# Performance work log

Hardware: AMD Instinct MI355X
Metric: run time of the kernel (lower is better)

Reference implementation:

```python
import jax, jax.numpy as jnp
import numpy as np
from jax import lax

B, L = 8, 2048
TOP_K = 30
NUM_RBF = 16
NUM_POS = 16
NODE_IN, EDGE_IN = 6, NUM_POS + NUM_RBF  # features_type='dist'
H = 128  # node_features == edge_features


def setup_inputs() -> dict:
    key = jax.random.key(0)
    ks = jax.random.split(key, 4)
    # coords scaled so pairwise distances span the RBF range [0, 20]
    X = jax.random.normal(ks[0], (B, L, 4, 3), dtype=jnp.float32) * 10.0
    mask = jnp.ones((B, L), dtype=jnp.float32)
    W_node = jax.random.normal(ks[1], (NODE_IN, H), dtype=jnp.float32) * 0.1
    b_node = jnp.zeros((H,), dtype=jnp.float32)
    W_edge = jax.random.normal(ks[2], (EDGE_IN, H), dtype=jnp.float32) * 0.1
    b_edge = jnp.zeros((H,), dtype=jnp.float32)
    gamma_n = jnp.ones((H,), dtype=jnp.float32)
    beta_n = jnp.zeros((H,), dtype=jnp.float32)
    gamma_e = jnp.ones((H,), dtype=jnp.float32)
    beta_e = jnp.zeros((H,), dtype=jnp.float32)
    return {"X": X, "mask": mask, "W_node": W_node, "b_node": b_node,
            "W_edge": W_edge, "b_edge": b_edge, "gamma_n": gamma_n,
            "beta_n": beta_n, "gamma_e": gamma_e, "beta_e": beta_e}


def _dist(X_ca, mask, eps=1e-6):
    # masked pairwise Euclidean distances + kNN (smallest)
    mask_2D = mask[:, None, :] * mask[:, :, None]            # [B,L,L]
    dX = X_ca[:, None, :, :] - X_ca[:, :, None, :]           # [B,L,L,3]
    D = mask_2D * jnp.sqrt(jnp.sum(dX * dX, axis=-1) + eps)  # [B,L,L]
    D_max = jnp.max(D, axis=-1, keepdims=True)
    D_adjust = D + (1.0 - mask_2D) * (D_max + 1.0)
    neg_D, E_idx = lax.top_k(-D_adjust, TOP_K)               # smallest-k
    return -neg_D, E_idx                                     # [B,L,K], [B,L,K]


def _rbf(D):
    D_mu = jnp.linspace(0.0, 20.0, NUM_RBF)                  # [R]
    D_sigma = 20.0 / NUM_RBF
    return jnp.exp(-(((D[..., None] - D_mu) / D_sigma) ** 2))  # [B,L,K,R]


def _positional_encodings(E_idx):
    # directional differential positional encodings
    N_nodes = E_idx.shape[1]
    ii = jnp.arange(N_nodes, dtype=jnp.float32)[None, :, None]
    d = (E_idx.astype(jnp.float32) - ii)[..., None]          # [B,L,K,1]
    freq = jnp.exp(jnp.arange(0, NUM_POS, 2, dtype=jnp.float32)
                   * (-(np.log(10000.0) / NUM_POS)))          # [P/2]
    angles = d * freq                                        # [B,L,K,P/2]
    return jnp.concatenate([jnp.cos(angles), jnp.sin(angles)], axis=-1)


def _dihedrals(X, eps=1e-7):
    # phi/psi/omega from N,CA,C backbone trace -> [B,L,6]
    b, n = X.shape[0], X.shape[1]
    Xb = X[:, :, :3, :].reshape(b, 3 * n, 3)
    dX = Xb[:, 1:, :] - Xb[:, :-1, :]
    U = dX / (jnp.linalg.norm(dX, axis=-1, keepdims=True) + 1e-8)
    u_2, u_1, u_0 = U[:, :-2], U[:, 1:-1], U[:, 2:]
    n_2 = jnp.cross(u_2, u_1)
    n_2 = n_2 / (jnp.linalg.norm(n_2, axis=-1, keepdims=True) + 1e-8)
    n_1 = jnp.cross(u_1, u_0)
    n_1 = n_1 / (jnp.linalg.norm(n_1, axis=-1, keepdims=True) + 1e-8)
    cosD = jnp.clip(jnp.sum(n_2 * n_1, axis=-1), -1.0 + eps, 1.0 - eps)
    Dang = jnp.sign(jnp.sum(u_2 * n_1, axis=-1)) * jnp.arccos(cosD)
    Dang = jnp.pad(Dang, ((0, 0), (1, 2)))
    Dang = Dang.reshape(b, n, 3)
    return jnp.concatenate([jnp.cos(Dang), jnp.sin(Dang)], axis=-1)


def _layer_norm(x, gamma, beta, eps=1e-5):
    mu = jnp.mean(x, axis=-1, keepdims=True)
    var = jnp.mean((x - mu) ** 2, axis=-1, keepdims=True)
    return (x - mu) * lax.rsqrt(var + eps) * gamma + beta


def reference(X, mask, W_node, b_node, W_edge, b_edge,
              gamma_n, beta_n, gamma_e, beta_e):
    X_ca = X[:, :, 1, :]
    D_neighbors, E_idx = _dist(X_ca, mask)
    E_positional = _positional_encodings(E_idx)              # [B,L,K,P]
    RBF = _rbf(D_neighbors)                                  # [B,L,K,R]
    V = _dihedrals(X)                                        # [B,L,6]
    E = jnp.concatenate([E_positional, RBF], axis=-1)        # [B,L,K,P+R]
    V = _layer_norm(V @ W_node + b_node, gamma_n, beta_n)
    E = _layer_norm(E @ W_edge + b_edge, gamma_e, beta_e)
    return V, E, E_idx
```

## Files before the change

### kernel.cpp

```cpp
#include <hip/hip_runtime.h>
#include <cstdint>
#include <cstddef>

#define NB 8
#define NL 2048
#define TOPK 30
#define NH 128
#define CAND_CAP 256
#define EDGE_BLOCKS 1920
#define EDGE_WAVES (EDGE_BLOCKS * 4)

typedef unsigned long long ull;
typedef __attribute__((ext_vector_type(8))) short short8v;
typedef __attribute__((ext_vector_type(4))) float f32x4;

__device__ __forceinline__ short f2bf(float f) {
    unsigned int b = __float_as_uint(f);
    b += 0x7fffu + ((b >> 16) & 1u);
    return (short)(b >> 16);
}

__global__ __launch_bounds__(512) void topk_kernel(
    const float* __restrict__ X, const float* __restrict__ mask,
    float* __restrict__ eidx, float* __restrict__ dnb)
{
    __shared__ float4 Ps[NL];
    __shared__ ull cand[8][CAND_CAP];

    const int tid = threadIdx.x;
    const int wv  = tid >> 6;
    const int ln  = tid & 63;
    const int row = blockIdx.x * 8 + wv;
    const int b   = row >> 11;
    const int i   = row & (NL - 1);

    const float* Xb = X + (size_t)b * NL * 12;
    const float* Mb = mask + (size_t)b * NL;
    #pragma unroll
    for (int q = 0; q < 4; ++q) {
        const int j = tid + 512 * q;
        const float* x = Xb + (size_t)j * 12 + 3;
        Ps[j] = make_float4(x[0], x[1], x[2], Mb[j]);
    }
    __syncthreads();

    const float4 pi = Ps[i];
    const float xi = pi.x, yi = pi.y, zi = pi.z, mi = pi.w;

    unsigned int u[32];
    float lm0 = 0.0f, lm1 = 0.0f, lm2 = 0.0f, lm3 = 0.0f;
    #pragma unroll
    for (int t = 0; t < 32; t += 4) {
        #pragma unroll
        for (int q = 0; q < 4; ++q) {
            const float4 pj = Ps[ln + 64 * (t + q)];
            float dx = xi - pj.x;
            float dy = yi - pj.y;
            float dz = zi - pj.z;
            float s = __fadd_rn(__fmul_rn(dx, dx), __fmul_rn(dy, dy));
            s = __fadd_rn(s, __fmul_rn(dz, dz));
            s = __fadd_rn(s, 1e-6f);
            float m2 = __fmul_rn(pj.w, mi);
            float d  = __fmul_rn(m2, __fsqrt_rn(s));
            u[t + q] = __float_as_uint(d) | ((m2 == 0.0f) ? 0x80000000u : 0u);
            if      (q == 0) lm0 = fmaxf(lm0, d);
            else if (q == 1) lm1 = fmaxf(lm1, d);
            else if (q == 2) lm2 = fmaxf(lm2, d);
            else             lm3 = fmaxf(lm3, d);
        }
    }
    float lmax = fmaxf(fmaxf(lm0, lm1), fmaxf(lm2, lm3));
    #pragma unroll
    for (int off = 32; off; off >>= 1) lmax = fmaxf(lmax, __shfl_xor(lmax, off));
    const unsigned int DMB = __float_as_uint(__fadd_rn(lmax, 1.0f));

    unsigned int um0 = 0xFFFFFFFFu, um1 = 0xFFFFFFFFu,
                 um2 = 0xFFFFFFFFu, um3 = 0xFFFFFFFFu;
    #pragma unroll
    for (int t = 0; t < 32; t += 4) {
        unsigned int b0 = (u[t+0] & 0x80000000u) ? DMB : u[t+0];
        unsigned int b1 = (u[t+1] & 0x80000000u) ? DMB : u[t+1];
        unsigned int b2 = (u[t+2] & 0x80000000u) ? DMB : u[t+2];
        unsigned int b3 = (u[t+3] & 0x80000000u) ? DMB : u[t+3];
        u[t+0] = b0; u[t+1] = b1; u[t+2] = b2; u[t+3] = b3;
        um0 = min(um0, b0); um1 = min(um1, b1);
        um2 = min(um2, b2); um3 = min(um3, b3);
    }
    unsigned int umin = min(min(um0, um1), min(um2, um3));

    unsigned int v = umin;
    #pragma unroll
    for (int k = 2; k <= 64; k <<= 1) {
        #pragma unroll
        for (int j = k >> 1; j > 0; j >>= 1) {
            unsigned int o = __shfl_xor(v, j);
            bool asc   = ((ln & k) == 0);
            bool lower = ((ln & j) == 0);
            v = (lower == asc) ? min(v, o) : max(v, o);
        }
    }
    const unsigned int T = __shfl(v, TOPK - 1);

    unsigned int base = 0;
    #pragma unroll
    for (int t = 0; t < 32; ++t) {
        bool act = u[t] <= T;
        ull m = __ballot(act);
        if (act) {
            unsigned int pos = base + (unsigned)__popcll(m & ((1ull << ln) - 1ull));
            if (pos < CAND_CAP)
                cand[wv][pos] = ((ull)u[t] << 32) | (unsigned)(ln + 64 * t);
        }
        base += (unsigned)__popcll(m);
    }
    const unsigned int cnt = base;

    float* eo  = eidx + (size_t)row * TOPK;
    float* dno = dnb  + (size_t)row * TOPK;

    if (cnt <= CAND_CAP) {
        ull k0 = ((unsigned)ln        < cnt) ? cand[wv][ln]        : ~0ULL;
        ull k1 = ((unsigned)ln +  64u < cnt) ? cand[wv][ln +  64]  : ~0ULL;
        ull k2 = ((unsigned)ln + 128u < cnt) ? cand[wv][ln + 128]  : ~0ULL;
        ull k3 = ((unsigned)ln + 192u < cnt) ? cand[wv][ln + 192]  : ~0ULL;
        int r0 = 0, r1 = 0, r2 = 0, r3 = 0;
        for (unsigned int p = 0; p < cnt; p += 4) {
            ull c0 = cand[wv][p];
            ull c1 = (p + 1 < cnt) ? cand[wv][p + 1] : ~0ULL;
            ull c2 = (p + 2 < cnt) ? cand[wv][p + 2] : ~0ULL;
            ull c3 = (p + 3 < cnt) ? cand[wv][p + 3] : ~0ULL;
            r0 += (c0 < k0) + (c1 < k0) + (c2 < k0) + (c3 < k0);
            r1 += (c0 < k1) + (c1 < k1) + (c2 < k1) + (c3 < k1);
            r2 += (c0 < k2) + (c1 < k2) + (c2 < k2) + (c3 < k2);
            r3 += (c0 < k3) + (c1 < k3) + (c2 < k3) + (c3 < k3);
        }
        if (r0 < TOPK) { eo[r0] = (float)(unsigned)(k0 & 0xFFFFFFFFu); dno[r0] = __uint_as_float((unsigned)(k0 >> 32)); }
        if (r1 < TOPK) { eo[r1] = (float)(unsigned)(k1 & 0xFFFFFFFFu); dno[r1] = __uint_as_float((unsigned)(k1 >> 32)); }
        if (r2 < TOPK) { eo[r2] = (float)(unsigned)(k2 & 0xFFFFFFFFu); dno[r2] = __uint_as_float((unsigned)(k2 >> 32)); }
        if (r3 < TOPK) { eo[r3] = (float)(unsigned)(k3 & 0xFFFFFFFFu); dno[r3] = __uint_as_float((unsigned)(k3 >> 32)); }
    } else {
        ull last = 0ULL;
        for (int k = 0; k < TOPK; ++k) {
            ull best = ~0ULL;
            #pragma unroll
            for (int t = 0; t < 32; ++t) {
                ull key = ((ull)u[t] << 32) | (unsigned)(ln + 64 * t);
                if (key > last && key < best) best = key;
            }
            #pragma unroll
            for (int off = 32; off; off >>= 1) {
                ull o = __shfl_xor(best, off);
                if (o < best) best = o;
            }
            if (ln == 0) {
                eo[k]  = (float)(unsigned)(best & 0xFFFFFFFFu);
                dno[k] = __uint_as_float((unsigned)(best >> 32));
            }
            last = best;
        }
    }
}

__global__ __launch_bounds__(256) void edge_vn_kernel(
    const float* __restrict__ eidx, const float* __restrict__ dnb,
    const float* __restrict__ We, const float* __restrict__ be,
    const float* __restrict__ ge, const float* __restrict__ bte,
    float* __restrict__ E,
    const float* __restrict__ X,  const float* __restrict__ Wn,
    const float* __restrict__ bn, const float* __restrict__ gn,
    const float* __restrict__ btn, float* __restrict__ V)
{
    __shared__ float shmem[4 * 16 * 132];

    const int tid  = threadIdx.x;
    const int lane = tid & 63;
    const int wv   = tid >> 6;

    if (blockIdx.x < EDGE_BLOCKS) {
        float (*ebuf)[132] = (float(*)[132])(shmem + wv * 16 * 132);
        const int c = lane & 15;
        const int g = lane >> 4;
        const int wid = blockIdx.x * 4 + wv;

        short8v W[8];
        #pragma unroll
        for (int t = 0; t < 8; ++t)
            #pragma unroll
            for (int e = 0; e < 8; ++e)
                W[t][e] = f2bf(We[(g * 8 + e) * NH + t * 16 + c]);

        float fcs[8];
        #pragma unroll
        for (int e = 0; e < 8; ++e) {
            if (g < 2) fcs[e] = expf((float)(2 * e) * -0.57564627f);
            else       fcs[e] = (float)((g - 2) * 8 + e) * (20.0f / 15.0f);
        }

        const int ntiles = NB * NL * TOPK / 16;
        for (int tile = wid; tile < ntiles; tile += EDGE_WAVES) {
            const int e0   = tile * 16;
            const int edge = e0 + c;
            const float fidx = eidx[edge];
            const float Dv   = dnb[edge];
            const int   row  = edge / TOPK;
            const float d    = fidx - (float)(row & (NL - 1));

            short8v F;
            if (g == 0) {
                #pragma unroll
                for (int e = 0; e < 8; ++e) F[e] = f2bf(cosf(d * fcs[e]));
            } else if (g == 1) {
                #pragma unroll
                for (int e = 0; e < 8; ++e) F[e] = f2bf(sinf(d * fcs[e]));
            } else {
                #pragma unroll
                for (int e = 0; e < 8; ++e) {
                    float tt = (Dv - fcs[e]) * 0.8f;
                    F[e] = f2bf(expf(-tt * tt));
                }
            }

            f32x4 acc[8];
            const f32x4 zero = {0.0f, 0.0f, 0.0f, 0.0f};
            #pragma unroll
            for (int t = 0; t < 8; ++t)
                acc[t] = __builtin_amdgcn_mfma_f32_16x16x32_bf16(W[t], F, zero, 0, 0, 0);

            float s = 0.0f, s2 = 0.0f;
            #pragma unroll
            for (int t = 0; t < 8; ++t) {
                const f32x4 b4 = *(const f32x4*)&be[t * 16 + g * 4];
                #pragma unroll
                for (int j = 0; j < 4; ++j) {
                    float vv = acc[t][j] + b4[j];
                    acc[t][j] = vv;
                    s  += vv;
                    s2 = fmaf(vv, vv, s2);
                }
            }
            s  += __shfl_xor(s, 16);  s  += __shfl_xor(s, 32);
            s2 += __shfl_xor(s2, 16); s2 += __shfl_xor(s2, 32);
            const float mean = s * (1.0f / 128.0f);
            const float var  = fmaxf(s2 * (1.0f / 128.0f) - mean * mean, 0.0f);
            const float inv  = rsqrtf(var + 1e-5f);

            #pragma unroll
            for (int t = 0; t < 8; ++t) {
                const f32x4 g4  = *(const f32x4*)&ge [t * 16 + g * 4];
                const f32x4 bt4 = *(const f32x4*)&bte[t * 16 + g * 4];
                f32x4 o;
                #pragma unroll
                for (int j = 0; j < 4; ++j)
                    o[j] = (acc[t][j] - mean) * inv * g4[j] + bt4[j];
                *(f32x4*)&ebuf[c][t * 16 + g * 4] = o;
            }

            float* const Ebase = E + (size_t)e0 * NH;
            #pragma unroll
            for (int q = 0; q < 8; ++q) {
                const int fi = q * 256 + lane * 4;
                const int ce = fi >> 7;
                const int id = fi & 127;
                const f32x4 o = *(const f32x4*)&ebuf[ce][id];
                __builtin_nontemporal_store(o, (f32x4*)&Ebase[(size_t)ce * NH + id]);
            }
        }
        return;
    }

    float (*fsh)[8] = (float(*)[8])shmem;
    const int node_base = (blockIdx.x - EDGE_BLOCKS) * 64;

    if (tid < 64) {
        const int ln   = tid;
        const int node = node_base + ln;
        const int b = node >> 11, i = node & (NL - 1);

        const int h0 = ln, h1 = ln + 64;
        float w0[6], w1[6];
        #pragma unroll
        for (int j = 0; j < 6; ++j) { w0[j] = Wn[j * NH + h0]; w1[j] = Wn[j * NH + h1]; }
        const float bb0 = bn[h0], bb1 = bn[h1];

        float st[35];
        {
            int idx = 0;
            #pragma unroll
            for (int j = 0; j < 6; ++j)
                #pragma unroll
                for (int k = j; k < 6; ++k)
                    st[idx++] = w0[j] * w0[k] + w1[j] * w1[k];
            #pragma unroll
            for (int j = 0; j < 6; ++j) st[21 + j] = w0[j] * bb0 + w1[j] * bb1;
            #pragma unroll
            for (int j = 0; j < 6; ++j) st[27 + j] = w0[j] + w1[j];
            st[33] = bb0 + bb1;
            st[34] = bb0 * bb0 + bb1 * bb1;
            #pragma unroll
            for (int q = 0; q < 35; ++q) {
                float vv = st[q];
                #pragma unroll
                for (int off = 32; off; off >>= 1) vv += __shfl_xor(vv, off);
                st[q] = vv;
            }
        }

        const float* XB = X + (size_t)b * NL * 12;
        const int rm1 = (i >= 1) ? i - 1 : 0;
        const int rp1 = (i <= NL - 2) ? i + 1 : NL - 1;
        float p[6][3];
        {
            const int rows[6]  = { rm1, i, i, i, rp1, rp1 };
            const int atoms[6] = { 2,   0, 1, 2, 0,   1   };
            #pragma unroll
            for (int k = 0; k < 6; ++k) {
                const float* q = XB + ((size_t)rows[k] * 4 + atoms[k]) * 3;
                p[k][0] = q[0]; p[k][1] = q[1]; p[k][2] = q[2];
            }
        }
        float uv[5][3], nv[4][3];
        #pragma unroll
        for (int k = 0; k < 5; ++k) {
            float vx = p[k+1][0] - p[k][0];
            float vy = p[k+1][1] - p[k][1];
            float vz = p[k+1][2] - p[k][2];
            float n = sqrtf(vx*vx + vy*vy + vz*vz) + 1e-8f;
            uv[k][0] = vx / n; uv[k][1] = vy / n; uv[k][2] = vz / n;
        }
        #pragma unroll
        for (int k = 0; k < 4; ++k) {
            float cx = uv[k][1]*uv[k+1][2] - uv[k][2]*uv[k+1][1];
            float cy = uv[k][2]*uv[k+1][0] - uv[k][0]*uv[k+1][2];
            float cz = uv[k][0]*uv[k+1][1] - uv[k][1]*uv[k+1][0];
            float n = sqrtf(cx*cx + cy*cy + cz*cz) + 1e-8f;
            nv[k][0] = cx / n; nv[k][1] = cy / n; nv[k][2] = cz / n;
        }
        float f[6];
        #pragma unroll
        for (int a = 0; a < 3; ++a) {
            bool valid = (a == 0) ? (i >= 1) : (i <= NL - 2);
            float cosD = nv[a][0]*nv[a+1][0] + nv[a][1]*nv[a+1][1] + nv[a][2]*nv[a+1][2];
            cosD = fminf(fmaxf(cosD, -1.0f + 1e-7f), 1.0f - 1e-7f);
            float sg = uv[a][0]*nv[a+1][0] + uv[a][1]*nv[a+1][1] + uv[a][2]*nv[a+1][2];
            float sgn = (sg > 0.0f) ? 1.0f : ((sg < 0.0f) ? -1.0f : 0.0f);
            float an = valid ? (sgn * acosf(cosD)) : 0.0f;
            f[a]     = cosf(an);
            f[3 + a] = sinf(an);
        }

        float s1 = st[33];
        #pragma unroll
        for (int j = 0; j < 6; ++j) s1 = fmaf(f[j], st[27 + j], s1);
        float qd = st[34];
        #pragma unroll
        for (int j = 0; j < 6; ++j) qd = fmaf(2.0f * f[j], st[21 + j], qd);
        {
            int idx = 0;
            #pragma unroll
            for (int j = 0; j < 6; ++j)
                #pragma unroll
                for (int k = j; k < 6; ++k) {
                    float coef = (j == k) ? 1.0f : 2.0f;
                    qd = fmaf(coef * f[j] * f[k], st[idx], qd);
                    ++idx;
                }
        }
        const float mean = s1 * (1.0f / 128.0f);
        const float var  = fmaxf(qd * (1.0f / 128.0f) - mean * mean, 0.0f);
        const float inv  = rsqrtf(var + 1e-5f);

        #pragma unroll
        for (int j = 0; j < 6; ++j) fsh[ln][j] = f[j];
        fsh[ln][6] = mean;
        fsh[ln][7] = inv;
    }
    __syncthreads();

    const int m  = tid & 31;
    const int ng = tid >> 5;
    const int h4 = m * 4;
    f32x4 w4[6];
    #pragma unroll
    for (int j = 0; j < 6; ++j) w4[j] = *(const f32x4*)&Wn[j * NH + h4];
    const f32x4 b4  = *(const f32x4*)&bn [h4];
    const f32x4 g4  = *(const f32x4*)&gn [h4];
    const f32x4 bt4 = *(const f32x4*)&btn[h4];

    #pragma unroll
    for (int it = 0; it < 8; ++it) {
        const int nn = it * 8 + ng;
        const float* fr = fsh[nn];
        f32x4 a = b4;
        #pragma unroll
        for (int j = 0; j < 6; ++j) {
            const float fj = fr[j];
            #pragma unroll
            for (int x = 0; x < 4; ++x) a[x] = fmaf(fj, w4[j][x], a[x]);
        }
        const float mn = fr[6], iv = fr[7];
        f32x4 o;
        #pragma unroll
        for (int x = 0; x < 4; ++x) o[x] = (a[x] - mn) * iv * g4[x] + bt4[x];
        *(f32x4*)&V[(size_t)(node_base + nn) * NH + h4] = o;
    }
}

extern "C" void kernel_launch(void* const* d_in, const int* in_sizes, int n_in,
                              void* d_out, int out_size, void* d_ws, size_t ws_size,
                              hipStream_t stream)
{
    const float* X    = (const float*)d_in[0];
    const float* mask = (const float*)d_in[1];
    const float* Wn   = (const float*)d_in[2];
    const float* bn   = (const float*)d_in[3];
    const float* We   = (const float*)d_in[4];
    const float* be   = (const float*)d_in[5];
    const float* gn   = (const float*)d_in[6];
    const float* btn  = (const float*)d_in[7];
    const float* ge   = (const float*)d_in[8];
    const float* bte  = (const float*)d_in[9];

    float* out = (float*)d_out;
    float* V   = out;
    float* E   = V  + (size_t)NB * NL * NH;
    float* EI  = E  + (size_t)NB * NL * TOPK * NH;

    float* dnb = (float*)d_ws;

    hipLaunchKernelGGL(topk_kernel,    dim3(NB * NL / 8),      dim3(512), 0, stream,
                       X, mask, EI, dnb);
    hipLaunchKernelGGL(edge_vn_kernel, dim3(EDGE_BLOCKS + 256), dim3(256), 0, stream,
                       EI, dnb, We, be, ge, bte, E, X, Wn, bn, gn, btn, V);
}
```

Baseline: 113.4 us.

## Recompute distances instead of caching in registers to raise topk occupancy

The top-k kernel no longer keeps 32 per-lane distances in a register array. It recomputes them from the shared-memory coordinates during candidate compaction and in the fallback path, and tracks the masked minimum during the first pass. It also halves the candidate buffer, sets a min-blocks launch bound, and skips ballot bookkeeping when no lane matches. The aim is lower VGPR and LDS use so more waves fit per CU, at the cost of doing the sqrt work twice and falling back to the slow selection path more often if candidate counts exceed 128.

```diff
diff --git a/kernel.cpp b/kernel.cpp
--- a/kernel.cpp
+++ b/kernel.cpp
@@ -6,7 +6,7 @@
 #define NL 2048
 #define TOPK 30
 #define NH 128
-#define CAND_CAP 256
+#define CAND_CAP 128
 #define EDGE_BLOCKS 1920
 #define EDGE_WAVES (EDGE_BLOCKS * 4)
 
@@ -20,7 +20,21 @@
     return (short)(b >> 16);
 }
 
-__global__ __launch_bounds__(512) void topk_kernel(
+__device__ __forceinline__ void dist_point(const float4 pj,
+                                           float xi, float yi, float zi, float mi,
+                                           float& d, bool& in) {
+    float dx = xi - pj.x;
+    float dy = yi - pj.y;
+    float dz = zi - pj.z;
+    float s = __fadd_rn(__fmul_rn(dx, dx), __fmul_rn(dy, dy));
+    s = __fadd_rn(s, __fmul_rn(dz, dz));
+    s = __fadd_rn(s, 1e-6f);
+    float m2 = __fmul_rn(pj.w, mi);
+    d  = __fmul_rn(m2, __fsqrt_rn(s));
+    in = (m2 != 0.0f);
+}
+
+__global__ __launch_bounds__(512, 8) void topk_kernel(
     const float* __restrict__ X, const float* __restrict__ mask,
     float* __restrict__ eidx, float* __restrict__ dnb)
 {
@@ -47,22 +61,15 @@
     const float4 pi = Ps[i];
     const float xi = pi.x, yi = pi.y, zi = pi.z, mi = pi.w;
 
-    unsigned int u[32];
     float lm0 = 0.0f, lm1 = 0.0f, lm2 = 0.0f, lm3 = 0.0f;
+    unsigned int umin_in = 0xFFFFFFFFu;
     #pragma unroll
     for (int t = 0; t < 32; t += 4) {
         #pragma unroll
         for (int q = 0; q < 4; ++q) {
-            const float4 pj = Ps[ln + 64 * (t + q)];
-            float dx = xi - pj.x;
-            float dy = yi - pj.y;
-            float dz = zi - pj.z;
-            float s = __fadd_rn(__fmul_rn(dx, dx), __fmul_rn(dy, dy));
-            s = __fadd_rn(s, __fmul_rn(dz, dz));
-            s = __fadd_rn(s, 1e-6f);
-            float m2 = __fmul_rn(pj.w, mi);
-            float d  = __fmul_rn(m2, __fsqrt_rn(s));
-            u[t + q] = __float_as_uint(d) | ((m2 == 0.0f) ? 0x80000000u : 0u);
+            float d; bool in;
+            dist_point(Ps[ln + 64 * (t + q)], xi, yi, zi, mi, d, in);
+            if (in) umin_in = min(umin_in, __float_as_uint(d));
             if      (q == 0) lm0 = fmaxf(lm0, d);
             else if (q == 1) lm1 = fmaxf(lm1, d);
             else if (q == 2) lm2 = fmaxf(lm2, d);
@@ -73,20 +80,7 @@
     #pragma unroll
     for (int off = 32; off; off >>= 1) lmax = fmaxf(lmax, __shfl_xor(lmax, off));
     const unsigned int DMB = __float_as_uint(__fadd_rn(lmax, 1.0f));
-
-    unsigned int um0 = 0xFFFFFFFFu, um1 = 0xFFFFFFFFu,
-                 um2 = 0xFFFFFFFFu, um3 = 0xFFFFFFFFu;
-    #pragma unroll
-    for (int t = 0; t < 32; t += 4) {
-        unsigned int b0 = (u[t+0] & 0x80000000u) ? DMB : u[t+0];
-        unsigned int b1 = (u[t+1] & 0x80000000u) ? DMB : u[t+1];
-        unsigned int b2 = (u[t+2] & 0x80000000u) ? DMB : u[t+2];
-        unsigned int b3 = (u[t+3] & 0x80000000u) ? DMB : u[t+3];
-        u[t+0] = b0; u[t+1] = b1; u[t+2] = b2; u[t+3] = b3;
-        um0 = min(um0, b0); um1 = min(um1, b1);
-        um2 = min(um2, b2); um3 = min(um3, b3);
-    }
-    unsigned int umin = min(min(um0, um1), min(um2, um3));
+    const unsigned int umin = min(umin_in, DMB);
 
     unsigned int v = umin;
     #pragma unroll
@@ -104,14 +98,19 @@
     unsigned int base = 0;
     #pragma unroll
     for (int t = 0; t < 32; ++t) {
-        bool act = u[t] <= T;
+        float d; bool in;
+        dist_point(Ps[ln + 64 * t], xi, yi, zi, mi, d, in);
+        const unsigned int adj = in ? __float_as_uint(d) : DMB;
+        const bool act = adj <= T;
         ull m = __ballot(act);
-        if (act) {
-            unsigned int pos = base + (unsigned)__popcll(m & ((1ull << ln) - 1ull));
-            if (pos < CAND_CAP)
-                cand[wv][pos] = ((ull)u[t] << 32) | (unsigned)(ln + 64 * t);
-        }
-        base += (unsigned)__popcll(m);
+        if (m) {
+            if (act) {
+                unsigned int pos = base + (unsigned)__popcll(m & ((1ull << ln) - 1ull));
+                if (pos < CAND_CAP)
+                    cand[wv][pos] = ((ull)adj << 32) | (unsigned)(ln + 64 * t);
+            }
+            base += (unsigned)__popcll(m);
+        }
     }
     const unsigned int cnt = base;
 
@@ -119,11 +118,9 @@
     float* dno = dnb  + (size_t)row * TOPK;
 
     if (cnt <= CAND_CAP) {
-        ull k0 = ((unsigned)ln        < cnt) ? cand[wv][ln]        : ~0ULL;
-        ull k1 = ((unsigned)ln +  64u < cnt) ? cand[wv][ln +  64]  : ~0ULL;
-        ull k2 = ((unsigned)ln + 128u < cnt) ? cand[wv][ln + 128]  : ~0ULL;
-        ull k3 = ((unsigned)ln + 192u < cnt) ? cand[wv][ln + 192]  : ~0ULL;
-        int r0 = 0, r1 = 0, r2 = 0, r3 = 0;
+        ull k0 = ((unsigned)ln       < cnt) ? cand[wv][ln]      : ~0ULL;
+        ull k1 = ((unsigned)ln + 64u < cnt) ? cand[wv][ln + 64] : ~0ULL;
+        int r0 = 0, r1 = 0;
         for (unsigned int p = 0; p < cnt; p += 4) {
             ull c0 = cand[wv][p];
             ull c1 = (p + 1 < cnt) ? cand[wv][p + 1] : ~0ULL;
@@ -131,20 +128,19 @@
             ull c3 = (p + 3 < cnt) ? cand[wv][p + 3] : ~0ULL;
             r0 += (c0 < k0) + (c1 < k0) + (c2 < k0) + (c3 < k0);
             r1 += (c0 < k1) + (c1 < k1) + (c2 < k1) + (c3 < k1);
-            r2 += (c0 < k2) + (c1 < k2) + (c2 < k2) + (c3 < k2);
-            r3 += (c0 < k3) + (c1 < k3) + (c2 < k3) + (c3 < k3);
         }
         if (r0 < TOPK) { eo[r0] = (float)(unsigned)(k0 & 0xFFFFFFFFu); dno[r0] = __uint_as_float((unsigned)(k0 >> 32)); }
         if (r1 < TOPK) { eo[r1] = (float)(unsigned)(k1 & 0xFFFFFFFFu); dno[r1] = __uint_as_float((unsigned)(k1 >> 32)); }
-        if (r2 < TOPK) { eo[r2] = (float)(unsigned)(k2 & 0xFFFFFFFFu); dno[r2] = __uint_as_float((unsigned)(k2 >> 32)); }
-        if (r3 < TOPK) { eo[r3] = (float)(unsigned)(k3 & 0xFFFFFFFFu); dno[r3] = __uint_as_float((unsigned)(k3 >> 32)); }
     } else {
         ull last = 0ULL;
         for (int k = 0; k < TOPK; ++k) {
             ull best = ~0ULL;
             #pragma unroll
             for (int t = 0; t < 32; ++t) {
-                ull key = ((ull)u[t] << 32) | (unsigned)(ln + 64 * t);
+                float d; bool in;
+                dist_point(Ps[ln + 64 * t], xi, yi, zi, mi, d, in);
+                const unsigned int adj = in ? __float_as_uint(d) : DMB;
+                ull key = ((ull)adj << 32) | (unsigned)(ln + 64 * t);
                 if (key > last && key < best) best = key;
             }
             #pragma unroll
@@ -427,7 +423,7 @@
 
     float* dnb = (float*)d_ws;
 
-    hipLaunchKernelGGL(topk_kernel,    dim3(NB * NL / 8),      dim3(512), 0, stream,
+    hipLaunchKernelGGL(topk_kernel,    dim3(NB * NL / 8),       dim3(512), 0, stream,
                        X, mask, EI, dnb);
     hipLaunchKernelGGL(edge_vn_kernel, dim3(EDGE_BLOCKS + 256), dim3(256), 0, stream,
                        EI, dnb, We, be, ge, bte, E, X, Wn, bn, gn, btn, V);
```

After: 126.5 us. +11.6%, slower.
